# Kernel tuning notes

Measured on AMD Instinct MI355X. Metric: run time of the kernel, lower is better.

Reference implementation:

```python
import jax, jax.numpy as jnp
import numpy as np

N_NODES = 50000
N_EDGES = 800000
NFEAT, NHID, NCLASS = 128, 256, 64


def setup_inputs() -> dict:
    key = jax.random.key(0)
    ks = jax.random.split(key, 8)
    x = jax.random.normal(ks[0], (N_NODES, NFEAT), dtype=jnp.float32)
    edge_index = jax.random.randint(ks[1], (2, N_EDGES), 0, N_NODES, dtype=jnp.int64)
    s1 = 1.0 / np.sqrt(NFEAT)
    s2 = 1.0 / np.sqrt(NHID)
    W1_neigh = jax.random.normal(ks[2], (NFEAT, NHID), dtype=jnp.float32) * s1
    W1_root = jax.random.normal(ks[3], (NFEAT, NHID), dtype=jnp.float32) * s1
    b1 = jnp.zeros((NHID,), dtype=jnp.float32)
    W2_neigh = jax.random.normal(ks[4], (NHID, NCLASS), dtype=jnp.float32) * s2
    W2_root = jax.random.normal(ks[5], (NHID, NCLASS), dtype=jnp.float32) * s2
    b2 = jnp.zeros((NCLASS,), dtype=jnp.float32)
    return {"x": x, "edge_index": edge_index, "W1_neigh": W1_neigh,
            "W1_root": W1_root, "b1": b1, "W2_neigh": W2_neigh,
            "W2_root": W2_root, "b2": b2}


def _sage_conv(h, src, dst, n_nodes, W_neigh, W_root, b):
    # mean aggregation of source features into destination nodes
    msg = h[src]                                                   # [E, d]
    summed = jax.ops.segment_sum(msg, dst, num_segments=n_nodes)   # [N, d]
    cnt = jax.ops.segment_sum(jnp.ones((src.shape[0],), h.dtype), dst,
                              num_segments=n_nodes)                # [N]
    mean = summed / jnp.maximum(cnt, 1.0)[:, None]
    return mean @ W_neigh + h @ W_root + b


def reference(x, edge_index, W1_neigh, W1_root, b1, W2_neigh, W2_root, b2):
    src, dst = edge_index[0], edge_index[1]
    n = x.shape[0]
    h = jax.nn.relu(_sage_conv(x, src, dst, n, W1_neigh, W1_root, b1))
    # dropout is identity in eval mode
    out = _sage_conv(h, src, dst, n, W2_neigh, W2_root, b2)
    return out
```

## Files before the change

### kernel.cpp

```cpp
#include <hip/hip_runtime.h>

#define N_NODES 50000
#define N_EDGES 800000
#define NFEAT   128
#define NHID    256
#define NCLASS  64

#define ELLCAP  64

#define NBUCK   56
#define BWIDTH  896
#define BCAP    16384
#define BIN_CH  4096
#define BIN_B   ((N_EDGES + BIN_CH - 1) / BIN_CH)
#define NFINE   ((N_NODES + 127) / 128)
#define FPB     7

#define CVTX_B  ((N_NODES * 32 + 255) / 256)
#define CVTW_B  (((65536 + 32768) + 255) / 256)

typedef unsigned short u16;
typedef unsigned int   u32;
typedef __attribute__((ext_vector_type(8))) short s16x8;
typedef __attribute__((ext_vector_type(4))) float f32x4;

__device__ inline u16 f2bf(float f) {
    u32 u = __float_as_uint(f);
    u32 r = (u + 0x7FFFu + ((u >> 16) & 1u)) >> 16;
    return (u16)r;
}
__device__ inline float bflo(u32 v) { return __uint_as_float(v << 16); }
__device__ inline float bfhi(u32 v) { return __uint_as_float(v & 0xFFFF0000u); }

#define GLOAD_LDS16(g, l)                                                        \
    __builtin_amdgcn_global_load_lds(                                            \
        (const __attribute__((address_space(1))) u32*)(const void*)(g),          \
        (__attribute__((address_space(3))) u32*)(void*)(l), 16, 0, 0)

__global__ __launch_bounds__(256) void prep_kernel(const float* __restrict__ x,
                                                   const int* __restrict__ ei,
                                                   const float* __restrict__ W1r,
                                                   const float* __restrict__ W1n,
                                                   const float* __restrict__ W2n,
                                                   const float* __restrict__ W2r,
                                                   u16* __restrict__ xa,
                                                   u32* __restrict__ gcnt,
                                                   u32* __restrict__ bbuf,
                                                   u16* __restrict__ W1t,
                                                   u16* __restrict__ W2t) {
    int b = blockIdx.x;
    if (b < BIN_B) {
        __shared__ u32 hist[NBUCK];
        __shared__ u32 base[NBUCK];
        int tid = threadIdx.x;
        if (tid < NBUCK) hist[tid] = 0;
        __syncthreads();
        u32 ek[16]; u32 rk[16]; int bk[16];
        int i0 = b * BIN_CH;
        #pragma unroll
        for (int k = 0; k < 16; ++k) {
            int i = i0 + k * 256 + tid;
            bk[k] = -1;
            if (i < N_EDGES) {
                u32 s = (u32)ei[i];
                u32 d = (u32)ei[N_EDGES + i];
                int bu = (int)(d / BWIDTH);
                ek[k] = (d << 16) | s;
                bk[k] = bu;
                rk[k] = atomicAdd(&hist[bu], 1u);
            }
        }
        __syncthreads();
        if (tid < NBUCK) base[tid] = atomicAdd(&gcnt[tid], hist[tid]);
        __syncthreads();
        #pragma unroll
        for (int k = 0; k < 16; ++k) {
            if (bk[k] >= 0) {
                u32 pos = base[bk[k]] + rk[k];
                if (pos < BCAP) bbuf[((u32)bk[k] << 14) + pos] = ek[k];
            }
        }
    } else if (b < BIN_B + CVTX_B) {
        int idx = (b - BIN_B) * 256 + threadIdx.x;
        if (idx >= N_NODES * 32) return;
        int r  = idx >> 5;
        int c4 = (idx & 31) * 4;
        float4 v = *reinterpret_cast<const float4*>(x + (size_t)r * NFEAT + c4);
        uint2 o;
        o.x = (u32)f2bf(v.x) | ((u32)f2bf(v.y) << 16);
        o.y = (u32)f2bf(v.z) | ((u32)f2bf(v.w) << 16);
        *reinterpret_cast<uint2*>(xa + (size_t)r * 256 + c4) = o;
    } else {
        int id = (b - BIN_B - CVTX_B) * 256 + threadIdx.x;
        if (id < 65536) {
            int k = id & 255, n = id >> 8;
            float v = (k < NFEAT) ? W1r[(size_t)k * NHID + n]
                                  : W1n[(size_t)(k - NFEAT) * NHID + n];
            W1t[(size_t)n * 256 + k] = f2bf(v);
        } else if (id < 65536 + 32768) {
            int j = id - 65536;
            int k = j & 255, n = j >> 8;
            float v = (n < NCLASS) ? W2n[(size_t)k * NCLASS + n]
                                   : W2r[(size_t)k * NCLASS + (n - NCLASS)];
            W2t[(size_t)n * 256 + k] = f2bf(v);
        }
    }
}

__global__ __launch_bounds__(512) void ell_build_kernel(const u32* __restrict__ bbuf,
                                                        const u32* __restrict__ gcnt,
                                                        int* __restrict__ cnt,
                                                        u16* __restrict__ ell) {
    __shared__ u32 hist[128];
    int tid = threadIdx.x;
    int f   = blockIdx.x;
    int cb  = f / FPB;
    int n0  = f * 128;
    if (tid < 128) hist[tid] = 0;
    __syncthreads();
    int m = (int)gcnt[cb]; if (m > BCAP) m = BCAP;
    const u32* bk = bbuf + ((u32)cb << 14);
    int i = tid;
    for (; i + 1536 < m; i += 2048) {
        u32 e0 = bk[i], e1 = bk[i + 512], e2 = bk[i + 1024], e3 = bk[i + 1536];
        u32 d0 = (e0 >> 16) - (u32)n0, d1 = (e1 >> 16) - (u32)n0;
        u32 d2 = (e2 >> 16) - (u32)n0, d3 = (e3 >> 16) - (u32)n0;
        if (d0 < 128u) { u32 p = atomicAdd(&hist[d0], 1u); if (p < ELLCAP) ell[(size_t)(n0 + (int)d0) * ELLCAP + p] = (u16)e0; }
        if (d1 < 128u) { u32 p = atomicAdd(&hist[d1], 1u); if (p < ELLCAP) ell[(size_t)(n0 + (int)d1) * ELLCAP + p] = (u16)e1; }
        if (d2 < 128u) { u32 p = atomicAdd(&hist[d2], 1u); if (p < ELLCAP) ell[(size_t)(n0 + (int)d2) * ELLCAP + p] = (u16)e2; }
        if (d3 < 128u) { u32 p = atomicAdd(&hist[d3], 1u); if (p < ELLCAP) ell[(size_t)(n0 + (int)d3) * ELLCAP + p] = (u16)e3; }
    }
    for (; i < m; i += 512) {
        u32 e = bk[i];
        u32 d = (e >> 16) - (u32)n0;
        if (d < 128u) { u32 p = atomicAdd(&hist[d], 1u); if (p < ELLCAP) ell[(size_t)(n0 + (int)d) * ELLCAP + p] = (u16)e; }
    }
    __syncthreads();
    if (tid < 128) cnt[n0 + tid] = (int)hist[tid];
}

#define ACC8(v)                                                      \
    do { a[0] += bflo((v).x); a[1] += bfhi((v).x);                   \
         a[2] += bflo((v).y); a[3] += bfhi((v).y);                   \
         a[4] += bflo((v).z); a[5] += bfhi((v).z);                   \
         a[6] += bflo((v).w); a[7] += bfhi((v).w); } while (0)

__global__ __launch_bounds__(256) void gather1_kernel(const int* __restrict__ cnt,
                                                      const u16* __restrict__ ell,
                                                      u16* __restrict__ xa) {
    int gtid = blockIdx.x * 256 + threadIdx.x;
    int node = gtid >> 6;
    if (node >= N_NODES) return;
    int lane = threadIdx.x & 63;
    int g = lane >> 4, lr = lane & 15;
    const u32* xrow = reinterpret_cast<const u32*>(xa);
    const u16* idx = ell + (size_t)node * ELLCAP;
    int deg = cnt[node];
    if (deg > ELLCAP) deg = ELLCAP;
    float a[8] = {};
    int j = 0;
    for (; j + 16 <= deg; j += 16) {
        int s0 = idx[j + g], s1 = idx[j + 4 + g], s2 = idx[j + 8 + g], s3 = idx[j + 12 + g];
        uint4 v0 = *reinterpret_cast<const uint4*>(xrow + (size_t)s0 * 128 + lr * 4);
        uint4 v1 = *reinterpret_cast<const uint4*>(xrow + (size_t)s1 * 128 + lr * 4);
        uint4 v2 = *reinterpret_cast<const uint4*>(xrow + (size_t)s2 * 128 + lr * 4);
        uint4 v3 = *reinterpret_cast<const uint4*>(xrow + (size_t)s3 * 128 + lr * 4);
        ACC8(v0); ACC8(v1); ACC8(v2); ACC8(v3);
    }
    for (; j + 4 <= deg; j += 4) {
        int s0 = idx[j + g];
        uint4 v0 = *reinterpret_cast<const uint4*>(xrow + (size_t)s0 * 128 + lr * 4);
        ACC8(v0);
    }
    if (g < deg - j) {
        int s0 = idx[j + g];
        uint4 v0 = *reinterpret_cast<const uint4*>(xrow + (size_t)s0 * 128 + lr * 4);
        ACC8(v0);
    }
    #pragma unroll
    for (int k = 0; k < 8; ++k) {
        a[k] += __shfl_xor(a[k], 16);
        a[k] += __shfl_xor(a[k], 32);
    }
    if (g == 0) {
        float invd = 1.0f / fmaxf((float)deg, 1.0f);
        uint4 pk;
        pk.x = (u32)f2bf(a[0] * invd) | ((u32)f2bf(a[1] * invd) << 16);
        pk.y = (u32)f2bf(a[2] * invd) | ((u32)f2bf(a[3] * invd) << 16);
        pk.z = (u32)f2bf(a[4] * invd) | ((u32)f2bf(a[5] * invd) << 16);
        pk.w = (u32)f2bf(a[6] * invd) | ((u32)f2bf(a[7] * invd) << 16);
        *reinterpret_cast<uint4*>(reinterpret_cast<u32*>(xa) + (size_t)node * 128 + 64 + lr * 4) = pk;
    }
}

__global__ __launch_bounds__(256) void gather2_kernel(const int* __restrict__ cnt,
                                                      const u16* __restrict__ ell,
                                                      const u16* __restrict__ t,
                                                      float* __restrict__ out) {
    int gtid = blockIdx.x * 256 + threadIdx.x;
    int node = gtid >> 6;
    if (node >= N_NODES) return;
    int lane = threadIdx.x & 63;
    int g = lane >> 3, lr = lane & 7;
    const u32* trow = reinterpret_cast<const u32*>(t);
    const u16* idx = ell + (size_t)node * ELLCAP;
    int deg = cnt[node];
    if (deg > ELLCAP) deg = ELLCAP;
    float a[8] = {};
    int j = 0;
    for (; j + 16 <= deg; j += 16) {
        int s0 = idx[j + g], s1 = idx[j + 8 + g];
        uint4 v0 = *reinterpret_cast<const uint4*>(trow + (size_t)s0 * 32 + lr * 4);
        uint4 v1 = *reinterpret_cast<const uint4*>(trow + (size_t)s1 * 32 + lr * 4);
        ACC8(v0); ACC8(v1);
    }
    for (; j + 8 <= deg; j += 8) {
        int s0 = idx[j + g];
        uint4 v0 = *reinterpret_cast<const uint4*>(trow + (size_t)s0 * 32 + lr * 4);
        ACC8(v0);
    }
    if (g < deg - j) {
        int s0 = idx[j + g];
        uint4 v0 = *reinterpret_cast<const uint4*>(trow + (size_t)s0 * 32 + lr * 4);
        ACC8(v0);
    }
    #pragma unroll
    for (int k = 0; k < 8; ++k) {
        a[k] += __shfl_xor(a[k], 8);
        a[k] += __shfl_xor(a[k], 16);
        a[k] += __shfl_xor(a[k], 32);
    }
    if (g == 0) {
        float invd = 1.0f / fmaxf((float)deg, 1.0f);
        float* o = out + (size_t)node * NCLASS + lr * 8;
        float4 o0 = *reinterpret_cast<float4*>(o);
        float4 o1 = *reinterpret_cast<float4*>(o + 4);
        o0.x += a[0] * invd; o0.y += a[1] * invd; o0.z += a[2] * invd; o0.w += a[3] * invd;
        o1.x += a[4] * invd; o1.y += a[5] * invd; o1.z += a[6] * invd; o1.w += a[7] * invd;
        *reinterpret_cast<float4*>(o) = o0;
        *reinterpret_cast<float4*>(o + 4) = o1;
    }
}

__global__ __launch_bounds__(256) void gemm1_mfma(const u16* __restrict__ xa,
                                                  const u16* __restrict__ W1t,
                                                  const float* __restrict__ b1,
                                                  u16* __restrict__ h) {
    __shared__ u16 As[128 * 32];
    __shared__ u16 Bs[128 * 32];
    const int tid = threadIdx.x;
    const int r0 = blockIdx.x * 128;
    const int n0 = blockIdx.y * 128;
    const int wid = tid >> 6, ln = tid & 63;
    const int wm = (wid & 1) * 64, wn = (wid >> 1) * 64;
    const int lr = ln & 15;
    const int lq = ln >> 4;

    f32x4 acc[4][4] = {};

    for (int k0 = 0; k0 < 256; k0 += 32) {
        #pragma unroll
        for (int it = 0; it < 2; ++it) {
            int c   = it * 256 + tid;
            int row = c >> 2;
            int ko  = (c & 3) * 8;
            GLOAD_LDS16(xa  + (size_t)(r0 + row) * 256 + k0 + ko, As + c * 8);
            GLOAD_LDS16(W1t + (size_t)(n0 + row) * 256 + k0 + ko, Bs + c * 8);
        }
        __syncthreads();

        s16x8 af[4], bf[4];
        #pragma unroll
        for (int i = 0; i < 4; ++i)
            af[i] = *reinterpret_cast<const s16x8*>(As + (wm + i * 16 + lr) * 32 + lq * 8);
        #pragma unroll
        for (int j = 0; j < 4; ++j)
            bf[j] = *reinterpret_cast<const s16x8*>(Bs + (wn + j * 16 + lr) * 32 + lq * 8);
        #pragma unroll
        for (int i = 0; i < 4; ++i)
            #pragma unroll
            for (int j = 0; j < 4; ++j)
                acc[i][j] = __builtin_amdgcn_mfma_f32_16x16x32_bf16(af[i], bf[j], acc[i][j], 0, 0, 0);
        __syncthreads();
    }

    #pragma unroll
    for (int i = 0; i < 4; ++i) {
        #pragma unroll
        for (int j = 0; j < 4; ++j) {
            int col = n0 + wn + j * 16 + lr;
            float bias = b1[col];
            #pragma unroll
            for (int r = 0; r < 4; ++r) {
                int row = r0 + wm + i * 16 + lq * 4 + r;
                if (row < N_NODES)
                    h[(size_t)row * 256 + col] = f2bf(fmaxf(acc[i][j][r] + bias, 0.0f));
            }
        }
    }
}

__global__ __launch_bounds__(256) void gemm2_mfma(const u16* __restrict__ h,
                                                  const u16* __restrict__ W2t,
                                                  const float* __restrict__ b2,
                                                  u16* __restrict__ t,
                                                  float* __restrict__ out) {
    __shared__ u16 As[128 * 32];
    __shared__ u16 Bs[128 * 32];
    const int tid = threadIdx.x;
    const int r0 = blockIdx.x * 128;
    const int wid = tid >> 6, ln = tid & 63;
    const int wm = (wid & 1) * 64, wn = (wid >> 1) * 64;
    const int lr = ln & 15;
    const int lq = ln >> 4;

    f32x4 acc[4][4] = {};

    for (int k0 = 0; k0 < 256; k0 += 32) {
        #pragma unroll
        for (int it = 0; it < 2; ++it) {
            int c   = it * 256 + tid;
            int row = c >> 2;
            int ko  = (c & 3) * 8;
            GLOAD_LDS16(h   + (size_t)(r0 + row) * 256 + k0 + ko, As + c * 8);
            GLOAD_LDS16(W2t + (size_t)row * 256 + k0 + ko,        Bs + c * 8);
        }
        __syncthreads();

        s16x8 af[4], bf[4];
        #pragma unroll
        for (int i = 0; i < 4; ++i)
            af[i] = *reinterpret_cast<const s16x8*>(As + (wm + i * 16 + lr) * 32 + lq * 8);
        #pragma unroll
        for (int j = 0; j < 4; ++j)
            bf[j] = *reinterpret_cast<const s16x8*>(Bs + (wn + j * 16 + lr) * 32 + lq * 8);
        #pragma unroll
        for (int i = 0; i < 4; ++i)
            #pragma unroll
            for (int j = 0; j < 4; ++j)
                acc[i][j] = __builtin_amdgcn_mfma_f32_16x16x32_bf16(af[i], bf[j], acc[i][j], 0, 0, 0);
        __syncthreads();
    }

    #pragma unroll
    for (int i = 0; i < 4; ++i) {
        #pragma unroll
        for (int j = 0; j < 4; ++j) {
            int col = wn + j * 16 + lr;
            #pragma unroll
            for (int r = 0; r < 4; ++r) {
                int row = r0 + wm + i * 16 + lq * 4 + r;
                if (row >= N_NODES) continue;
                if (col < NCLASS) {
                    t[(size_t)row * NCLASS + col] = f2bf(acc[i][j][r]);
                } else {
                    int c = col - NCLASS;
                    out[(size_t)row * NCLASS + c] = acc[i][j][r] + b2[c];
                }
            }
        }
    }
}

extern "C" void kernel_launch(void* const* d_in, const int* in_sizes, int n_in,
                              void* d_out, int out_size, void* d_ws, size_t ws_size,
                              hipStream_t stream) {
    const float* x    = (const float*)d_in[0];
    const int*   ei   = (const int*)d_in[1];
    const float* W1n  = (const float*)d_in[2];
    const float* W1r  = (const float*)d_in[3];
    const float* b1   = (const float*)d_in[4];
    const float* W2n  = (const float*)d_in[5];
    const float* W2r  = (const float*)d_in[6];
    const float* b2   = (const float*)d_in[7];
    float* out = (float*)d_out;

    u32* gcnt = (u32*)d_ws;
    u32* bbuf = gcnt + 64;
    int* cnt  = (int*)(bbuf + ((size_t)NBUCK << 14));
    u16* ell  = (u16*)(cnt + 50048);
    u16* xa   = ell + (size_t)N_NODES * ELLCAP;
    u16* h    = xa + (size_t)N_NODES * 256;
    u16* t    = h  + (size_t)N_NODES * 256;
    u16* W1t  = t  + (size_t)N_NODES * 64;
    u16* W2t  = W1t + 65536;

    hipMemsetAsync(gcnt, 0, 64 * sizeof(u32), stream);

    prep_kernel<<<BIN_B + CVTX_B + CVTW_B, 256, 0, stream>>>(
        x, ei, W1r, W1n, W2n, W2r, xa, gcnt, bbuf, W1t, W2t);
    ell_build_kernel<<<NFINE, 512, 0, stream>>>(bbuf, gcnt, cnt, ell);

    gather1_kernel<<<(N_NODES * 64 + 255) / 256, 256, 0, stream>>>(cnt, ell, xa);
    gemm1_mfma<<<dim3((N_NODES + 127) / 128, 2), 256, 0, stream>>>(xa, W1t, b1, h);

    gemm2_mfma<<<(N_NODES + 127) / 128, 256, 0, stream>>>(h, W2t, b2, t, out);
    gather2_kernel<<<(N_NODES * 64 + 255) / 256, 256, 0, stream>>>(cnt, ell, t, out);
}
```

Measured before the change: 204.2 us.

## Fuse layer-1 and layer-2 GEMMs, keeping hidden tile in shared memory

```diff
diff --git a/kernel.cpp b/kernel.cpp
--- a/kernel.cpp
+++ b/kernel.cpp
@@ -242,71 +242,16 @@
     }
 }
 
-__global__ __launch_bounds__(256) void gemm1_mfma(const u16* __restrict__ xa,
-                                                  const u16* __restrict__ W1t,
-                                                  const float* __restrict__ b1,
-                                                  u16* __restrict__ h) {
+__global__ __launch_bounds__(256) void gemm12_fused(const u16* __restrict__ xa,
+                                                    const u16* __restrict__ W1t,
+                                                    const float* __restrict__ b1,
+                                                    const u16* __restrict__ W2t,
+                                                    const float* __restrict__ b2,
+                                                    u16* __restrict__ t,
+                                                    float* __restrict__ out) {
     __shared__ u16 As[128 * 32];
     __shared__ u16 Bs[128 * 32];
-    const int tid = threadIdx.x;
-    const int r0 = blockIdx.x * 128;
-    const int n0 = blockIdx.y * 128;
-    const int wid = tid >> 6, ln = tid & 63;
-    const int wm = (wid & 1) * 64, wn = (wid >> 1) * 64;
-    const int lr = ln & 15;
-    const int lq = ln >> 4;
-
-    f32x4 acc[4][4] = {};
-
-    for (int k0 = 0; k0 < 256; k0 += 32) {
-        #pragma unroll
-        for (int it = 0; it < 2; ++it) {
-            int c   = it * 256 + tid;
-            int row = c >> 2;
-            int ko  = (c & 3) * 8;
-            GLOAD_LDS16(xa  + (size_t)(r0 + row) * 256 + k0 + ko, As + c * 8);
-            GLOAD_LDS16(W1t + (size_t)(n0 + row) * 256 + k0 + ko, Bs + c * 8);
-        }
-        __syncthreads();
-
-        s16x8 af[4], bf[4];
-        #pragma unroll
-        for (int i = 0; i < 4; ++i)
-            af[i] = *reinterpret_cast<const s16x8*>(As + (wm + i * 16 + lr) * 32 + lq * 8);
-        #pragma unroll
-        for (int j = 0; j < 4; ++j)
-            bf[j] = *reinterpret_cast<const s16x8*>(Bs + (wn + j * 16 + lr) * 32 + lq * 8);
-        #pragma unroll
-        for (int i = 0; i < 4; ++i)
-            #pragma unroll
-            for (int j = 0; j < 4; ++j)
-                acc[i][j] = __builtin_amdgcn_mfma_f32_16x16x32_bf16(af[i], bf[j], acc[i][j], 0, 0, 0);
-        __syncthreads();
-    }
-
-    #pragma unroll
-    for (int i = 0; i < 4; ++i) {
-        #pragma unroll
-        for (int j = 0; j < 4; ++j) {
-            int col = n0 + wn + j * 16 + lr;
-            float bias = b1[col];
-            #pragma unroll
-            for (int r = 0; r < 4; ++r) {
-                int row = r0 + wm + i * 16 + lq * 4 + r;
-                if (row < N_NODES)
-                    h[(size_t)row * 256 + col] = f2bf(fmaxf(acc[i][j][r] + bias, 0.0f));
-            }
-        }
-    }
-}
-
-__global__ __launch_bounds__(256) void gemm2_mfma(const u16* __restrict__ h,
-                                                  const u16* __restrict__ W2t,
-                                                  const float* __restrict__ b2,
-                                                  u16* __restrict__ t,
-                                                  float* __restrict__ out) {
-    __shared__ u16 As[128 * 32];
-    __shared__ u16 Bs[128 * 32];
+    __shared__ u16 hs[128 * 256];
     const int tid = threadIdx.x;
     const int r0 = blockIdx.x * 128;
     const int wid = tid >> 6, ln = tid & 63;
@@ -314,23 +259,65 @@
     const int lr = ln & 15;
     const int lq = ln >> 4;
 
+    #pragma unroll 1
+    for (int n0 = 0; n0 < 256; n0 += 128) {
+        f32x4 acc[4][4] = {};
+        for (int k0 = 0; k0 < 256; k0 += 32) {
+            #pragma unroll
+            for (int it = 0; it < 2; ++it) {
+                int c   = it * 256 + tid;
+                int row = c >> 2;
+                int ko  = (c & 3) * 8;
+                GLOAD_LDS16(xa  + (size_t)(r0 + row) * 256 + k0 + ko, As + c * 8);
+                GLOAD_LDS16(W1t + (size_t)(n0 + row) * 256 + k0 + ko, Bs + c * 8);
+            }
+            __syncthreads();
+
+            s16x8 af[4], bf[4];
+            #pragma unroll
+            for (int i = 0; i < 4; ++i)
+                af[i] = *reinterpret_cast<const s16x8*>(As + (wm + i * 16 + lr) * 32 + lq * 8);
+            #pragma unroll
+            for (int j = 0; j < 4; ++j)
+                bf[j] = *reinterpret_cast<const s16x8*>(Bs + (wn + j * 16 + lr) * 32 + lq * 8);
+            #pragma unroll
+            for (int i = 0; i < 4; ++i)
+                #pragma unroll
+                for (int j = 0; j < 4; ++j)
+                    acc[i][j] = __builtin_amdgcn_mfma_f32_16x16x32_bf16(af[i], bf[j], acc[i][j], 0, 0, 0);
+            __syncthreads();
+        }
+        #pragma unroll
+        for (int i = 0; i < 4; ++i) {
+            #pragma unroll
+            for (int j = 0; j < 4; ++j) {
+                int col = n0 + wn + j * 16 + lr;
+                float bias = b1[col];
+                #pragma unroll
+                for (int r = 0; r < 4; ++r) {
+                    int row = wm + i * 16 + lq * 4 + r;
+                    hs[row * 256 + (col ^ ((row & 7) << 3))] =
+                        f2bf(fmaxf(acc[i][j][r] + bias, 0.0f));
+                }
+            }
+        }
+    }
+
     f32x4 acc[4][4] = {};
-
     for (int k0 = 0; k0 < 256; k0 += 32) {
-        #pragma unroll
-        for (int it = 0; it < 2; ++it) {
-            int c   = it * 256 + tid;
-            int row = c >> 2;
-            int ko  = (c & 3) * 8;
-            GLOAD_LDS16(h   + (size_t)(r0 + row) * 256 + k0 + ko, As + c * 8);
-            GLOAD_LDS16(W2t + (size_t)row * 256 + k0 + ko,        Bs + c * 8);
+        {
+            int c0 = tid, c1 = 256 + tid;
+            GLOAD_LDS16(W2t + (size_t)(c0 >> 2) * 256 + k0 + (c0 & 3) * 8, Bs + c0 * 8);
+            GLOAD_LDS16(W2t + (size_t)(c1 >> 2) * 256 + k0 + (c1 & 3) * 8, Bs + c1 * 8);
         }
         __syncthreads();
 
         s16x8 af[4], bf[4];
         #pragma unroll
-        for (int i = 0; i < 4; ++i)
-            af[i] = *reinterpret_cast<const s16x8*>(As + (wm + i * 16 + lr) * 32 + lq * 8);
+        for (int i = 0; i < 4; ++i) {
+            int row = wm + i * 16 + lr;
+            af[i] = *reinterpret_cast<const s16x8*>(hs + row * 256 + ((k0 + lq * 8) ^ ((row & 7) << 3)));
+        }
         #pragma unroll
         for (int j = 0; j < 4; ++j)
             bf[j] = *reinterpret_cast<const s16x8*>(Bs + (wn + j * 16 + lr) * 32 + lq * 8);
@@ -380,8 +367,7 @@
     int* cnt  = (int*)(bbuf + ((size_t)NBUCK << 14));
     u16* ell  = (u16*)(cnt + 50048);
     u16* xa   = ell + (size_t)N_NODES * ELLCAP;
-    u16* h    = xa + (size_t)N_NODES * 256;
-    u16* t    = h  + (size_t)N_NODES * 256;
+    u16* t    = xa + (size_t)50048 * 256;
     u16* W1t  = t  + (size_t)N_NODES * 64;
     u16* W2t  = W1t + 65536;
 
@@ -392,8 +378,8 @@
     ell_build_kernel<<<NFINE, 512, 0, stream>>>(bbuf, gcnt, cnt, ell);
 
     gather1_kernel<<<(N_NODES * 64 + 255) / 256, 256, 0, stream>>>(cnt, ell, xa);
-    gemm1_mfma<<<dim3((N_NODES + 127) / 128, 2), 256, 0, stream>>>(xa, W1t, b1, h);
-
-    gemm2_mfma<<<(N_NODES + 127) / 128, 256, 0, stream>>>(h, W2t, b2, t, out);
+
+    gemm12_fused<<<NFINE, 256, 0, stream>>>(xa, W1t, b1, W2t, b2, t, out);
+
     gather2_kernel<<<(N_NODES * 64 + 255) / 256, 256, 0, stream>>>(cnt, ell, t, out);
 }
```

Result: faster. 191.7 us (median of 2 runs) (-6.1%).
